# Kernel optimization log

Measured on AMD Instinct MI355X. Metric: run time of the kernel, lower is better.

The kernel has to match this reference:

```python
import jax, jax.numpy as jnp
import numpy as np

ALPHA = 0.2      # LeakyReLU negative slope
NEG_BIG = -9e15  # mask value from the original module


def setup_inputs() -> dict:
    key = jax.random.key(0)
    kx, ka, kW, ka1, ka2, kb = jax.random.split(key, 6)
    B, N, F_in, F_out = 8, 2048, 256, 128
    x = jax.random.normal(kx, (B, N, F_in), dtype=jnp.float32)
    adj = (jax.random.uniform(ka, (B, N, N)) < 0.1).astype(jnp.float32)
    adj = adj.at[:, jnp.arange(N), jnp.arange(N)].set(1.0)
    # parameters (xavier-uniform-ish scaling)
    W = jax.random.normal(kW, (F_out, F_in), dtype=jnp.float32) * np.sqrt(2.0 / (F_in + F_out))
    a1 = jax.random.normal(ka1, (F_out,), dtype=jnp.float32) * np.sqrt(2.0 / (2 * F_out + 1))
    a2 = jax.random.normal(ka2, (F_out,), dtype=jnp.float32) * np.sqrt(2.0 / (2 * F_out + 1))
    a_b = jax.random.normal(kb, (1,), dtype=jnp.float32) * 0.01
    return {"x": x, "adj": adj, "W": W, "a1": a1, "a2": a2, "a_b": a_b}


def reference(x, adj, W, a1, a2, a_b):
    # h = W(input): [B, N, F_out]
    h = jnp.einsum('bnf,of->bno', x, W)
    # a([h_i, h_j]) == a1.h_i + a2.h_j + bias  (exact decomposition of the concat)
    s1 = h @ a1  # [B, N] contribution of row-repeated node i
    s2 = h @ a2  # [B, N] contribution of tiled node j
    e = jax.nn.leaky_relu(s1[:, :, None] + s2[:, None, :] + a_b[0], negative_slope=ALPHA)  # [B,N,N]
    att = jnp.where(adj > 0, e, NEG_BIG)
    att = jax.nn.softmax(att, axis=1)  # softmax over dim=1, as in the original
    # dropout is a no-op in eval mode
    att = att * adj
    h_prime = jnp.einsum('bij,bjo->bio', att, h)
    return jax.nn.elu(h_prime)  # concat=True -> ELU
```

## Files before the change

kernel.cpp:

```cpp
#include <hip/hip_runtime.h>
#include <stdint.h>

typedef unsigned int  uint32;
typedef unsigned long long u64;

#define L2E 1.44269504088896340736f

typedef float f32x4 __attribute__((ext_vector_type(4)));
typedef short bf16x8 __attribute__((ext_vector_type(8)));

__device__ __forceinline__ unsigned short f2bf(float f){
  uint32 u = __float_as_uint(f);
  u += 0x7fffu + ((u >> 16) & 1u);
  return (unsigned short)(u >> 16);
}


__global__ __launch_bounds__(256) void k_mask(const float* __restrict__ adj,
                                              u64* __restrict__ mask){
  const int lane = threadIdx.x & 63;
  const size_t t = (size_t)blockIdx.x * 256 + threadIdx.x;
  const f32x4* ap = (const f32x4*)adj;
  #pragma unroll 4
  for (int it = 0; it < 16; ++it){
    size_t n = (size_t)it * 524288 + t;
    f32x4 av = ap[n];
    u64 b0 = __ballot(av[0] != 0.f);
    u64 b1 = __ballot(av[1] != 0.f);
    u64 b2 = __ballot(av[2] != 0.f);
    u64 b3 = __ballot(av[3] != 0.f);
    if (lane == 0){
      size_t nb = n & ~(size_t)63;
      size_t row = nb >> 9;
      int c = (int)((nb >> 6) & 7);
      ulonglong2* dst = (ulonglong2*)(mask + row * 32 + c * 4);
      dst[0] = (ulonglong2){b0, b1};
      dst[1] = (ulonglong2){b2, b3};
    }
  }
}

__global__ __launch_bounds__(256) void k_h(const float* __restrict__ x,
                                           const float* __restrict__ W,
                                           const float* __restrict__ a1,
                                           const float* __restrict__ a2,
                                           const float* __restrict__ ab,
                                           float* __restrict__ h,
                                           float* __restrict__ E1,
                                           float* __restrict__ E2p){
  __shared__ unsigned short xs[2][64][72];
  __shared__ unsigned short wsm[2][128][72];
  const int tid = threadIdx.x;
  const int wv = tid >> 6, lane = tid & 63;
  const int r = lane & 15, kg = lane >> 4;
  const int row0 = blockIdx.x * 64;

  f32x4 acc[8];
  #pragma unroll
  for (int of = 0; of < 8; ++of) acc[of] = (f32x4){0.f,0.f,0.f,0.f};

  for (int kc = 0; kc < 4; ++kc){
    if (kc) __syncthreads();
    #pragma unroll
    for (int it = 0; it < 4; ++it){
      int idx = tid + it * 256;
      int row = idx >> 4, f = (idx & 15) * 4;
      float4 v = *(const float4*)(x + (size_t)(row0 + row) * 256 + kc * 64 + f);
      ushort4 hi, lo;
      { unsigned short hh = f2bf(v.x); float rr = v.x - __uint_as_float(((uint32)hh)<<16); hi.x = hh; lo.x = f2bf(rr); }
      { unsigned short hh = f2bf(v.y); float rr = v.y - __uint_as_float(((uint32)hh)<<16); hi.y = hh; lo.y = f2bf(rr); }
      { unsigned short hh = f2bf(v.z); float rr = v.z - __uint_as_float(((uint32)hh)<<16); hi.z = hh; lo.z = f2bf(rr); }
      { unsigned short hh = f2bf(v.w); float rr = v.w - __uint_as_float(((uint32)hh)<<16); hi.w = hh; lo.w = f2bf(rr); }
      *(ushort4*)&xs[0][row][f] = hi;
      *(ushort4*)&xs[1][row][f] = lo;
    }
    #pragma unroll
    for (int it = 0; it < 8; ++it){
      int idx = tid + it * 256;
      int o = idx >> 4, f = (idx & 15) * 4;
      float4 v = *(const float4*)(W + (size_t)o * 256 + kc * 64 + f);
      ushort4 hi, lo;
      { unsigned short hh = f2bf(v.x); float rr = v.x - __uint_as_float(((uint32)hh)<<16); hi.x = hh; lo.x = f2bf(rr); }
      { unsigned short hh = f2bf(v.y); float rr = v.y - __uint_as_float(((uint32)hh)<<16); hi.y = hh; lo.y = f2bf(rr); }
      { unsigned short hh = f2bf(v.z); float rr = v.z - __uint_as_float(((uint32)hh)<<16); hi.z = hh; lo.z = f2bf(rr); }
      { unsigned short hh = f2bf(v.w); float rr = v.w - __uint_as_float(((uint32)hh)<<16); hi.w = hh; lo.w = f2bf(rr); }
      *(ushort4*)&wsm[0][o][f] = hi;
      *(ushort4*)&wsm[1][o][f] = lo;
    }
    __syncthreads();
    #pragma unroll
    for (int kk = 0; kk < 2; ++kk){
      bf16x8 ah = *(const bf16x8*)&xs[0][wv*16 + r][kk*32 + kg*8];
      bf16x8 al = *(const bf16x8*)&xs[1][wv*16 + r][kk*32 + kg*8];
      #pragma unroll
      for (int of = 0; of < 8; ++of){
        bf16x8 bh = *(const bf16x8*)&wsm[0][of*16 + r][kk*32 + kg*8];
        bf16x8 bl = *(const bf16x8*)&wsm[1][of*16 + r][kk*32 + kg*8];
        acc[of] = __builtin_amdgcn_mfma_f32_16x16x32_bf16(ah, bh, acc[of], 0, 0, 0);
        acc[of] = __builtin_amdgcn_mfma_f32_16x16x32_bf16(ah, bl, acc[of], 0, 0, 0);
        acc[of] = __builtin_amdgcn_mfma_f32_16x16x32_bf16(al, bh, acc[of], 0, 0, 0);
      }
    }
  }
  #pragma unroll
  for (int of = 0; of < 8; ++of)
    #pragma unroll
    for (int q = 0; q < 4; ++q)
      h[(size_t)(row0 + wv*16 + kg*4 + q) * 128 + of*16 + r] = acc[of][q];

  float p1[4] = {0,0,0,0}, p2[4] = {0,0,0,0};
  #pragma unroll
  for (int of = 0; of < 8; ++of){
    float w1 = a1[of*16 + r], w2 = a2[of*16 + r];
    #pragma unroll
    for (int q = 0; q < 4; ++q){
      p1[q] = fmaf(acc[of][q], w1, p1[q]);
      p2[q] = fmaf(acc[of][q], w2, p2[q]);
    }
  }
  #pragma unroll
  for (int off = 8; off; off >>= 1)
    #pragma unroll
    for (int q = 0; q < 4; ++q){
      p1[q] += __shfl_xor(p1[q], off);
      p2[q] += __shfl_xor(p2[q], off);
    }
  if (r == 0){
    float abv = ab[0];
    #pragma unroll
    for (int q = 0; q < 4; ++q){
      int row = row0 + wv*16 + kg*4 + q;
      E1[row] = p1[q] * L2E;
      int bb = row >> 11, j = row & 2047;
      int kp = (j & ~255) + (j & 3) * 64 + ((j & 255) >> 2);
      E2p[bb * 2048 + kp] = (p2[q] + abv) * L2E;
    }
  }
}

__global__ __launch_bounds__(256) void k_den(const u64* __restrict__ mask,
                                             const float* __restrict__ E1,
                                             const float* __restrict__ E2p,
                                             float* __restrict__ denomK){
  const int wg = blockIdx.x, ch = blockIdx.y, b = blockIdx.z;
  const int wv = threadIdx.x >> 6, lane = threadIdx.x & 63;
  const int w = wg * 4 + wv;
  const float e2 = E2p[b * 2048 + w * 64 + lane];
  const u64 lmask = 1ull << lane;
  const float* e1p = E1 + b * 2048 + ch * 128;
  const u64* mpp = mask + (size_t)(b * 2048 + ch * 128) * 32 + w;

  float acc = 0.f;
  #pragma unroll 8
  for (int i = 0; i < 128; ++i){
    u64 wb = mpp[(size_t)i * 32];
    float e1 = e1p[i];
    float t = e1 + e2;
    t = fmaxf(t, 0.2f * t);
    float v = __builtin_amdgcn_exp2f(t);
    acc += (wb & lmask) ? v : 0.f;
  }
  denomK[(size_t)ch * 16384 + b * 2048 + w * 64 + lane] = acc;
}

__global__ __launch_bounds__(256) void k_gt(const float* __restrict__ h,
                                            const float* __restrict__ denomK,
                                            unsigned short* __restrict__ gTp){
  __shared__ float hl[8464];
  __shared__ float rrec[256];
  const int b = blockIdx.z, Q = blockIdx.x, ot = blockIdx.y;
  const int o0 = ot * 32;
  const int tid = threadIdx.x;

  {
    const int kpl = (tid & 3) * 64 + (tid >> 2);
    float d = 0.f;
    #pragma unroll
    for (int ch = 0; ch < 16; ++ch)
      d += denomK[(size_t)ch * 16384 + b * 2048 + Q * 256 + kpl];
    rrec[tid] = 1.0f / d;
  }
  __syncthreads();

  #pragma unroll
  for (int it = 0; it < 8; ++it){
    int idx = tid + it * 256;
    int j = idx >> 3, f = idx & 7;
    float4 v = *(const float4*)(h + (size_t)(b * 2048 + Q * 256 + j) * 128 + o0 + f * 4);
    float rc = rrec[j];
    int base = j * 33 + (j >> 4) + f * 4;
    hl[base + 0] = v.x * rc;
    hl[base + 1] = v.y * rc;
    hl[base + 2] = v.z * rc;
    hl[base + 3] = v.w * rc;
  }
  __syncthreads();

  const int u  = tid & 127;
  const int fh = tid >> 7;
  const int lane = u >> 1;
  const int e0 = (u & 1) * 4;
  const int orow_r = lane & 15;
  const int kgrp = lane >> 4;
  #pragma unroll
  for (int it = 0; it < 8; ++it){
    int f  = it * 2 + fh;
    int kb = f >> 1, sl = f & 1;
    int orow = sl * 16 + orow_r;
    int klb = kb * 32 + kgrp * 8 + e0;
    ushort4 uu;
    { int kl = klb + 0; int jl = 4 * (kl & 63) + (kl >> 6); uu.x = f2bf(hl[jl * 33 + (jl >> 4) + orow]); }
    { int kl = klb + 1; int jl = 4 * (kl & 63) + (kl >> 6); uu.y = f2bf(hl[jl * 33 + (jl >> 4) + orow]); }
    { int kl = klb + 2; int jl = 4 * (kl & 63) + (kl >> 6); uu.z = f2bf(hl[jl * 33 + (jl >> 4) + orow]); }
    { int kl = klb + 3; int jl = 4 * (kl & 63) + (kl >> 6); uu.w = f2bf(hl[jl * 33 + (jl >> 4) + orow]); }
    size_t dst = ((size_t)((b * 64 + Q * 8 + kb) * 8 + (ot * 2 + sl))) * 512 + lane * 8 + e0;
    *(ushort4*)(gTp + dst) = uu;
  }
}

__global__ __launch_bounds__(256) void k_main(const float* __restrict__ E1,
                                              const float* __restrict__ E2p,
                                              const uint32* __restrict__ mask32,
                                              const unsigned short* __restrict__ gTp,
                                              float* __restrict__ out){
  __shared__ float cmb[4][32][129];
  const int b  = blockIdx.y;
  const int ib = blockIdx.x;
  const int wv = threadIdx.x >> 6, lane = threadIdx.x & 63;
  const int r  = lane & 15, kg = lane >> 4;
  const int gi0 = b * 2048 + ib * 32 + r;
  const float e1_0 = E1[gi0];
  const float e1_1 = E1[gi0 + 16];
  const uint32* m0 = mask32 + (size_t)gi0 * 64;
  const uint32* m1 = mask32 + (size_t)(gi0 + 16) * 64;

  f32x4 acc[2][8];
  #pragma unroll
  for (int si = 0; si < 2; ++si)
    #pragma unroll
    for (int so = 0; so < 8; ++so)
      acc[si][so] = (f32x4){0.f, 0.f, 0.f, 0.f};

  const int k0 = wv * 512, k1 = k0 + 512;
  for (int kk = k0; kk < k1; kk += 32){
    const int j0 = kk + kg * 8;
    const float4 eA = *(const float4*)(E2p + b * 2048 + j0);
    const float4 eB = *(const float4*)(E2p + b * 2048 + j0 + 4);
    const uint32 bits0 = (m0[kk >> 5] >> (kg * 8)) & 0xffu;
    const uint32 bits1 = (m1[kk >> 5] >> (kg * 8)) & 0xffu;
    float e2v[8] = {eA.x, eA.y, eA.z, eA.w, eB.x, eB.y, eB.z, eB.w};

    union { uint32 u[4]; bf16x8 v; } af0, af1;
    #pragma unroll
    for (int p = 0; p < 4; ++p){
      {
        float t0 = e1_0 + e2v[2*p];     t0 = fmaxf(t0, 0.2f * t0);
        float t1 = e1_0 + e2v[2*p+1];   t1 = fmaxf(t1, 0.2f * t1);
        float x0 = ((bits0 >> (2*p))   & 1u) ? __builtin_amdgcn_exp2f(t0) : 0.f;
        float x1 = ((bits0 >> (2*p+1)) & 1u) ? __builtin_amdgcn_exp2f(t1) : 0.f;
        uint32 u0 = __float_as_uint(x0); u0 = (u0 + 0x7fffu + ((u0 >> 16) & 1u)) >> 16;
        uint32 u1 = __float_as_uint(x1); u1 = (u1 + 0x7fffu + ((u1 >> 16) & 1u)) & 0xffff0000u;
        af0.u[p] = u0 | u1;
      }
      {
        float t0 = e1_1 + e2v[2*p];     t0 = fmaxf(t0, 0.2f * t0);
        float t1 = e1_1 + e2v[2*p+1];   t1 = fmaxf(t1, 0.2f * t1);
        float x0 = ((bits1 >> (2*p))   & 1u) ? __builtin_amdgcn_exp2f(t0) : 0.f;
        float x1 = ((bits1 >> (2*p+1)) & 1u) ? __builtin_amdgcn_exp2f(t1) : 0.f;
        uint32 u0 = __float_as_uint(x0); u0 = (u0 + 0x7fffu + ((u0 >> 16) & 1u)) >> 16;
        uint32 u1 = __float_as_uint(x1); u1 = (u1 + 0x7fffu + ((u1 >> 16) & 1u)) & 0xffff0000u;
        af1.u[p] = u0 | u1;
      }
    }
    const unsigned short* gk = gTp + ((size_t)(b * 64 + (kk >> 5)) * 8) * 512 + lane * 8;
    #pragma unroll
    for (int so = 0; so < 8; ++so){
      bf16x8 bfr = *(const bf16x8*)(gk + so * 512);
      acc[0][so] = __builtin_amdgcn_mfma_f32_16x16x32_bf16(af0.v, bfr, acc[0][so], 0, 0, 0);
      acc[1][so] = __builtin_amdgcn_mfma_f32_16x16x32_bf16(af1.v, bfr, acc[1][so], 0, 0, 0);
    }
  }

  #pragma unroll
  for (int si = 0; si < 2; ++si)
    #pragma unroll
    for (int so = 0; so < 8; ++so)
      #pragma unroll
      for (int q = 0; q < 4; ++q){
        int il = si * 16 + kg * 4 + q;
        int o  = so * 16 + r;
        cmb[wv][il][o] = acc[si][so][q];
      }
  __syncthreads();
  for (int e = threadIdx.x; e < 4096; e += 256){
    int i = e >> 7, o = e & 127;
    float v = cmb[0][i][o] + cmb[1][i][o] + cmb[2][i][o] + cmb[3][i][o];
    float res = v > 0.f ? v : (__builtin_amdgcn_exp2f(v * L2E) - 1.0f);
    out[(size_t)(b * 2048 + ib * 32 + i) * 128 + o] = res;
  }
}

extern "C" void kernel_launch(void* const* d_in, const int* in_sizes, int n_in,
                              void* d_out, int out_size, void* d_ws, size_t ws_size,
                              hipStream_t stream){
  const float* x   = (const float*)d_in[0];
  const float* adj = (const float*)d_in[1];
  const float* W   = (const float*)d_in[2];
  const float* a1  = (const float*)d_in[3];
  const float* a2  = (const float*)d_in[4];
  const float* ab  = (const float*)d_in[5];
  float* out = (float*)d_out;

  const size_t WS_NEEDED = 17956864;
  if (ws_size < WS_NEEDED) return;

  char* ws = (char*)d_ws;
  float* h      = (float*)(ws);
  float* E1     = (float*)(ws + 8388608);
  float* E2p    = (float*)(ws + 8454144);
  float* denomK = (float*)(ws + 8519680);
  u64*   mask   = (u64*)  (ws + 9568256);
  unsigned short* gTp = (unsigned short*)(ws + 13762560);

  k_mask<<<2048, 256, 0, stream>>>(adj, mask);
  k_h   <<<256, 256, 0, stream>>>(x, W, a1, a2, ab, h, E1, E2p);
  k_den <<<dim3(8, 16, 8), 256, 0, stream>>>(mask, E1, E2p, denomK);
  k_gt  <<<dim3(8, 4, 8), 256, 0, stream>>>(h, denomK, gTp);
  k_main<<<dim3(64, 8), 256, 0, stream>>>(E1, E2p, (const uint32*)mask, gTp, out);
}
```

Measured before the change: 85.31 us.

## Replace ballot bitmask with per-thread nibble byte mask and adapt consumers

The adjacency mask is now built as one byte per float4 (4 bits) written directly by each thread, with no wavefront ballots and no lane-0 scattered stores. The denominator and main kernels are rewritten to read this byte layout: k_den processes four columns per thread over 64 rows with 32 partial chunks, and k_main loads 8 bytes per step and extracts bits. The mask doubles in size (4 bits per 4 entries stored in a byte), which adds memory traffic in exchange for a simpler, coalesced mask build.

```diff
diff --git a/kernel.cpp b/kernel.cpp
--- a/kernel.cpp
+++ b/kernel.cpp
@@ -3,6 +3,7 @@
 
 typedef unsigned int  uint32;
 typedef unsigned long long u64;
+typedef unsigned char u8;
 
 #define L2E 1.44269504088896340736f
 
@@ -16,27 +17,17 @@
 }
 
 
-__global__ __launch_bounds__(256) void k_mask(const float* __restrict__ adj,
-                                              u64* __restrict__ mask){
-  const int lane = threadIdx.x & 63;
+__global__ __launch_bounds__(256) void k_maskb(const float* __restrict__ adj,
+                                               u8* __restrict__ mb){
   const size_t t = (size_t)blockIdx.x * 256 + threadIdx.x;
   const f32x4* ap = (const f32x4*)adj;
-  #pragma unroll 4
+  #pragma unroll 8
   for (int it = 0; it < 16; ++it){
     size_t n = (size_t)it * 524288 + t;
     f32x4 av = ap[n];
-    u64 b0 = __ballot(av[0] != 0.f);
-    u64 b1 = __ballot(av[1] != 0.f);
-    u64 b2 = __ballot(av[2] != 0.f);
-    u64 b3 = __ballot(av[3] != 0.f);
-    if (lane == 0){
-      size_t nb = n & ~(size_t)63;
-      size_t row = nb >> 9;
-      int c = (int)((nb >> 6) & 7);
-      ulonglong2* dst = (ulonglong2*)(mask + row * 32 + c * 4);
-      dst[0] = (ulonglong2){b0, b1};
-      dst[1] = (ulonglong2){b2, b3};
-    }
+    uint32 bByte = (av[0] != 0.f ? 1u : 0u) | (av[1] != 0.f ? 2u : 0u)
+                 | (av[2] != 0.f ? 4u : 0u) | (av[3] != 0.f ? 8u : 0u);
+    mb[n] = (u8)bByte;
   }
 }
 
@@ -138,29 +129,42 @@
   }
 }
 
-__global__ __launch_bounds__(256) void k_den(const u64* __restrict__ mask,
+__global__ __launch_bounds__(256) void k_den(const u8* __restrict__ mb,
                                              const float* __restrict__ E1,
                                              const float* __restrict__ E2p,
                                              float* __restrict__ denomK){
-  const int wg = blockIdx.x, ch = blockIdx.y, b = blockIdx.z;
+  const int c = blockIdx.x, chb = blockIdx.y, b = blockIdx.z;
   const int wv = threadIdx.x >> 6, lane = threadIdx.x & 63;
-  const int w = wg * 4 + wv;
-  const float e2 = E2p[b * 2048 + w * 64 + lane];
-  const u64 lmask = 1ull << lane;
-  const float* e1p = E1 + b * 2048 + ch * 128;
-  const u64* mpp = mask + (size_t)(b * 2048 + ch * 128) * 32 + w;
-
-  float acc = 0.f;
+  const int ch32 = chb * 4 + wv;
+  const int gi0 = b * 2048 + ch32 * 64;
+
+  float e2v[4];
+  #pragma unroll
+  for (int p = 0; p < 4; ++p)
+    e2v[p] = E2p[b * 2048 + c * 256 + p * 64 + lane];
+
+  const float* e1p = E1 + gi0;
+  const u8* mp = mb + (size_t)gi0 * 512 + c * 64 + lane;
+
+  float ds0 = 0.f, ds1 = 0.f, ds2 = 0.f, ds3 = 0.f;
   #pragma unroll 8
-  for (int i = 0; i < 128; ++i){
-    u64 wb = mpp[(size_t)i * 32];
+  for (int i = 0; i < 64; ++i){
+    uint32 byte = mp[(size_t)i * 512];
     float e1 = e1p[i];
-    float t = e1 + e2;
-    t = fmaxf(t, 0.2f * t);
-    float v = __builtin_amdgcn_exp2f(t);
-    acc += (wb & lmask) ? v : 0.f;
-  }
-  denomK[(size_t)ch * 16384 + b * 2048 + w * 64 + lane] = acc;
+    float t0 = e1 + e2v[0]; t0 = fmaxf(t0, 0.2f * t0);
+    float t1 = e1 + e2v[1]; t1 = fmaxf(t1, 0.2f * t1);
+    float t2 = e1 + e2v[2]; t2 = fmaxf(t2, 0.2f * t2);
+    float t3 = e1 + e2v[3]; t3 = fmaxf(t3, 0.2f * t3);
+    ds0 += (byte & 1u) ? __builtin_amdgcn_exp2f(t0) : 0.f;
+    ds1 += (byte & 2u) ? __builtin_amdgcn_exp2f(t1) : 0.f;
+    ds2 += (byte & 4u) ? __builtin_amdgcn_exp2f(t2) : 0.f;
+    ds3 += (byte & 8u) ? __builtin_amdgcn_exp2f(t3) : 0.f;
+  }
+  float* dk = denomK + (size_t)ch32 * 16384 + b * 2048 + c * 256;
+  dk[0 * 64 + lane] = ds0;
+  dk[1 * 64 + lane] = ds1;
+  dk[2 * 64 + lane] = ds2;
+  dk[3 * 64 + lane] = ds3;
 }
 
 __global__ __launch_bounds__(256) void k_gt(const float* __restrict__ h,
@@ -176,7 +180,7 @@
     const int kpl = (tid & 3) * 64 + (tid >> 2);
     float d = 0.f;
     #pragma unroll
-    for (int ch = 0; ch < 16; ++ch)
+    for (int ch = 0; ch < 32; ++ch)
       d += denomK[(size_t)ch * 16384 + b * 2048 + Q * 256 + kpl];
     rrec[tid] = 1.0f / d;
   }
@@ -220,7 +224,7 @@
 
 __global__ __launch_bounds__(256) void k_main(const float* __restrict__ E1,
                                               const float* __restrict__ E2p,
-                                              const uint32* __restrict__ mask32,
+                                              const u8* __restrict__ mb,
                                               const unsigned short* __restrict__ gTp,
                                               float* __restrict__ out){
   __shared__ float cmb[4][32][129];
@@ -231,8 +235,8 @@
   const int gi0 = b * 2048 + ib * 32 + r;
   const float e1_0 = E1[gi0];
   const float e1_1 = E1[gi0 + 16];
-  const uint32* m0 = mask32 + (size_t)gi0 * 64;
-  const uint32* m1 = mask32 + (size_t)(gi0 + 16) * 64;
+  const u8* mrow0 = mb + (size_t)gi0 * 512 + kg * 8;
+  const u8* mrow1 = mb + (size_t)(gi0 + 16) * 512 + kg * 8;
 
   f32x4 acc[2][8];
   #pragma unroll
@@ -246,8 +250,10 @@
     const int j0 = kk + kg * 8;
     const float4 eA = *(const float4*)(E2p + b * 2048 + j0);
     const float4 eB = *(const float4*)(E2p + b * 2048 + j0 + 4);
-    const uint32 bits0 = (m0[kk >> 5] >> (kg * 8)) & 0xffu;
-    const uint32 bits1 = (m1[kk >> 5] >> (kg * 8)) & 0xffu;
+    const int boff = (kk >> 8) * 64 + (kk & 63);
+    const int pb = (kk >> 6) & 3;
+    const u64 mq0 = *(const u64*)(mrow0 + boff);
+    const u64 mq1 = *(const u64*)(mrow1 + boff);
     float e2v[8] = {eA.x, eA.y, eA.z, eA.w, eB.x, eB.y, eB.z, eB.w};
 
     union { uint32 u[4]; bf16x8 v; } af0, af1;
@@ -256,8 +262,8 @@
       {
         float t0 = e1_0 + e2v[2*p];     t0 = fmaxf(t0, 0.2f * t0);
         float t1 = e1_0 + e2v[2*p+1];   t1 = fmaxf(t1, 0.2f * t1);
-        float x0 = ((bits0 >> (2*p))   & 1u) ? __builtin_amdgcn_exp2f(t0) : 0.f;
-        float x1 = ((bits0 >> (2*p+1)) & 1u) ? __builtin_amdgcn_exp2f(t1) : 0.f;
+        float x0 = ((mq0 >> (2*p*8 + pb)) & 1ull) ? __builtin_amdgcn_exp2f(t0) : 0.f;
+        float x1 = ((mq0 >> ((2*p+1)*8 + pb)) & 1ull) ? __builtin_amdgcn_exp2f(t1) : 0.f;
         uint32 u0 = __float_as_uint(x0); u0 = (u0 + 0x7fffu + ((u0 >> 16) & 1u)) >> 16;
         uint32 u1 = __float_as_uint(x1); u1 = (u1 + 0x7fffu + ((u1 >> 16) & 1u)) & 0xffff0000u;
         af0.u[p] = u0 | u1;
@@ -265,8 +271,8 @@
       {
         float t0 = e1_1 + e2v[2*p];     t0 = fmaxf(t0, 0.2f * t0);
         float t1 = e1_1 + e2v[2*p+1];   t1 = fmaxf(t1, 0.2f * t1);
-        float x0 = ((bits1 >> (2*p))   & 1u) ? __builtin_amdgcn_exp2f(t0) : 0.f;
-        float x1 = ((bits1 >> (2*p+1)) & 1u) ? __builtin_amdgcn_exp2f(t1) : 0.f;
+        float x0 = ((mq1 >> (2*p*8 + pb)) & 1ull) ? __builtin_amdgcn_exp2f(t0) : 0.f;
+        float x1 = ((mq1 >> ((2*p+1)*8 + pb)) & 1ull) ? __builtin_amdgcn_exp2f(t1) : 0.f;
         uint32 u0 = __float_as_uint(x0); u0 = (u0 + 0x7fffu + ((u0 >> 16) & 1u)) >> 16;
         uint32 u1 = __float_as_uint(x1); u1 = (u1 + 0x7fffu + ((u1 >> 16) & 1u)) & 0xffff0000u;
         af1.u[p] = u0 | u1;
@@ -311,7 +317,7 @@
   const float* ab  = (const float*)d_in[5];
   float* out = (float*)d_out;
 
-  const size_t WS_NEEDED = 17956864;
+  const size_t WS_NEEDED = 23199744;
   if (ws_size < WS_NEEDED) return;
 
   char* ws = (char*)d_ws;
@@ -319,12 +325,12 @@
   float* E1     = (float*)(ws + 8388608);
   float* E2p    = (float*)(ws + 8454144);
   float* denomK = (float*)(ws + 8519680);
-  u64*   mask   = (u64*)  (ws + 9568256);
-  unsigned short* gTp = (unsigned short*)(ws + 13762560);
-
-  k_mask<<<2048, 256, 0, stream>>>(adj, mask);
-  k_h   <<<256, 256, 0, stream>>>(x, W, a1, a2, ab, h, E1, E2p);
-  k_den <<<dim3(8, 16, 8), 256, 0, stream>>>(mask, E1, E2p, denomK);
-  k_gt  <<<dim3(8, 4, 8), 256, 0, stream>>>(h, denomK, gTp);
-  k_main<<<dim3(64, 8), 256, 0, stream>>>(E1, E2p, (const uint32*)mask, gTp, out);
-}
+  u8*    maskB  = (u8*)   (ws + 10616832);
+  unsigned short* gTp = (unsigned short*)(ws + 19005440);
+
+  k_maskb<<<2048, 256, 0, stream>>>(adj, maskB);
+  k_h    <<<256, 256, 0, stream>>>(x, W, a1, a2, ab, h, E1, E2p);
+  k_den  <<<dim3(8, 8, 8), 256, 0, stream>>>(maskB, E1, E2p, denomK);
+  k_gt   <<<dim3(8, 4, 8), 256, 0, stream>>>(h, denomK, gTp);
+  k_main <<<dim3(64, 8), 256, 0, stream>>>(E1, E2p, maskB, gTp, out);
+}
```

Result: faster. 80.95 us (-5.1%).
